# Kernel optimization log

Hardware: AMD Instinct MI355X
Metric: run time of the kernel (lower is better)

The kernel has to match this reference:

```python
import jax, jax.numpy as jnp
import numpy as np

N = 30000   # clients (single instance, repeat=1)
F = 16      # num_node_features
EP = 30000  # solution-graph (tour) edges per parent
EF = 240000 # full graph k-NN edges (degree 8)
H = 8       # heads
D = 64      # hidden_dim
R = 64      # routes per parent (= max_to_move)
HD = H * D  # 512


def _gatv2(x, src, dst, ea, Wl, Wr, We, att, b, d_out):
    # PyG GATv2Conv: score = att . leaky_relu(Wl x_src + Wr x_dst + We e), softmax over dst
    n = x.shape[0]
    xl = (x @ Wl).reshape(n, H, d_out)
    xr = (x @ Wr).reshape(n, H, d_out)
    ee = (ea @ We).reshape(-1, H, d_out)
    s = jax.nn.leaky_relu(xl[src] + xr[dst] + ee, 0.2)          # [E,H,d]
    logits = jnp.einsum('ehd,hd->eh', s, att)                    # [E,H]
    m = jax.ops.segment_max(logits, dst, num_segments=n)
    ex = jnp.exp(logits - m[dst])
    den = jax.ops.segment_sum(ex, dst, num_segments=n)
    alpha = ex / (den[dst] + 1e-16)
    out = jax.ops.segment_sum(xl[src] * alpha[..., None], dst, num_segments=n)
    return out.reshape(n, H * d_out) + b


def _bn(x, g, b):
    # BatchNorm with track_running_stats=False -> batch statistics
    mu = jnp.mean(x, 0)
    v = jnp.var(x, 0)
    return (x - mu) * jax.lax.rsqrt(v + 1e-5) * g + b


def _routes(emb, rid):
    # sum client embeddings per route, then prefix sums over routes (moved vs kept sets)
    rs = jax.ops.segment_sum(emb, rid, num_segments=R)   # [R, 2HD]
    cs = jnp.cumsum(rs, 0)
    return cs, cs[-1] - cs


def setup_inputs() -> dict:
    key = jax.random.key(0)
    ks = iter(jax.random.split(key, 64))
    sc = 0.05
    rn = lambda shape: jax.random.normal(next(ks), shape, jnp.float32)
    d = {}
    d['x_p1'] = rn((N, F)); d['x_p2'] = rn((N, F)); d['x_full'] = rn((N, F))
    d['ea_p1'] = jax.random.uniform(next(ks), (EP, 1))
    d['ea_p2'] = jax.random.uniform(next(ks), (EP, 1))
    d['ea_full'] = jax.random.uniform(next(ks), (EF, 1))
    d['ei_p1'] = jax.random.randint(next(ks), (2, EP), 0, N)
    d['ei_p2'] = jax.random.randint(next(ks), (2, EP), 0, N)
    d['ei_full'] = jax.random.randint(next(ks), (2, EF), 0, N)
    d['route_p1'] = jax.random.randint(next(ks), (N,), 0, R)
    d['route_p2'] = jax.random.randint(next(ks), (N,), 0, R)
    # GAT params: (SolutionGraph, FullGraph, both)
    for tag, cin, dout in (('1', F, D), ('2', F, D), ('3', 2 * HD, 2 * D)):
        d['Wl' + tag] = rn((cin, H * dout)) * sc
        d['Wr' + tag] = rn((cin, H * dout)) * sc
        d['We' + tag] = rn((1, H * dout)) * sc
        d['att' + tag] = rn((H, dout)) * sc
        d['b' + tag] = jnp.zeros((H * dout,), jnp.float32)
    d['bng'] = jnp.ones((2 * HD,), jnp.float32); d['bnb'] = jnp.zeros((2 * HD,), jnp.float32)
    d['png'] = jnp.ones((8 * HD,), jnp.float32); d['pnb'] = jnp.zeros((8 * HD,), jnp.float32)
    dims = [8 * HD, 4 * HD, 2 * HD, HD, HD // 2, HD // 4, HD // 8, HD // 16, 1]
    for i in range(8):
        d['W%d' % (i + 1)] = rn((dims[i], dims[i + 1])) * sc
        d['c%d' % (i + 1)] = jnp.zeros((dims[i + 1],), jnp.float32)
    return d


def reference(x_p1, x_p2, x_full, ea_p1, ea_p2, ea_full, ei_p1, ei_p2, ei_full,
              route_p1, route_p2,
              Wl1, Wr1, We1, att1, b1, Wl2, Wr2, We2, att2, b2,
              Wl3, Wr3, We3, att3, b3, bng, bnb, png, pnb,
              W1, c1, W2, c2, W3, c3, W4, c4, W5, c5, W6, c6, W7, c7, W8, c8):
    p1 = _gatv2(x_p1, ei_p1[0], ei_p1[1], ea_p1, Wl1, Wr1, We1, att1, b1, D)
    p2 = _gatv2(x_p2, ei_p2[0], ei_p2[1], ea_p2, Wl1, Wr1, We1, att1, b1, D)
    fg = _gatv2(x_full, ei_full[0], ei_full[1], ea_full, Wl2, Wr2, We2, att2, b2, D)
    # single instance -> repeat=1: concat client embedding with full-graph embedding
    p1f = _bn(jnp.concatenate([p1, fg], 1), bng, bnb)
    p2f = _bn(jnp.concatenate([p2, fg], 1), bng, bnb)
    p1f = _gatv2(p1f, ei_p1[0], ei_p1[1], ea_p1, Wl3, Wr3, We3, att3, b3, 2 * D)
    p2f = _gatv2(p2f, ei_p2[0], ei_p2[1], ea_p2, Wl3, Wr3, We3, att3, b3, 2 * D)
    c1s, r1s = _routes(p1f, route_p1)
    c2s, r2s = _routes(p2f, route_p2)
    ptop = jnp.concatenate([c1s, r1s, c2s, r2s], 1)   # [R, 8*HD]
    h = _bn(ptop, png, pnb)
    lrelu = lambda z: jax.nn.leaky_relu(z, 0.01)
    h = lrelu(h @ W1 + c1)
    h = lrelu(h @ W2 + c2)
    h = lrelu(h @ W3 + c3)
    h = lrelu(h @ W4 + c4)
    h = lrelu(h @ W5 + c5)
    h = lrelu(h @ W6 + c6)
    h = lrelu(h @ W7 + c7)
    h = h @ W8 + c8
    probs = jax.nn.sigmoid(h).ravel()
    ptop_batch = jnp.zeros((R,), jnp.int32)
    return probs, ptop_batch
```

## Files before the change

### kernel.cpp

```cpp
#include <hip/hip_runtime.h>
#include <stdint.h>

typedef unsigned short u16;
typedef unsigned int   u32;
typedef __attribute__((ext_vector_type(8))) short bf16x8;
typedef __attribute__((ext_vector_type(4))) float f32x4;

#define NN    30000
#define EFULL 240000
#define EPAR  30000

__device__ __forceinline__ float b2f(u16 u){ u32 x=((u32)u)<<16; float f; __builtin_memcpy(&f,&x,4); return f; }
__device__ __forceinline__ u16 f2b(float f){ u32 x; __builtin_memcpy(&x,&f,4); x += 0x7fffu + ((x>>16)&1u); return (u16)(x>>16); }

__device__ __forceinline__ void gload_lds16(const u16* g, u16* l){
  __builtin_amdgcn_global_load_lds((const __attribute__((address_space(1))) void*)g,
                                   (__attribute__((address_space(3))) void*)l, 16, 0, 0);
}

__global__ void k_fail(float* out){ int t=threadIdx.x; if(t<128) out[t]=2.0f; }

__global__ void k_counte3(const int* __restrict__ d0, const int* __restrict__ d1, const int* __restrict__ d2,
                          int* __restrict__ c0, int* __restrict__ c1, int* __restrict__ c2){
  int z = blockIdx.z;
  const int* d = z==0? d0 : z==1? d1 : d2;
  int* c = z==0? c0 : z==1? c1 : c2;
  int E = z==0? EFULL : EPAR;
  int e = blockIdx.x*256 + threadIdx.x;
  if (e < E) atomicAdd(&c[d[e]], 1);
}

__global__ void k_scan3(const int* __restrict__ c0, const int* __restrict__ c1, const int* __restrict__ c2,
                        int* __restrict__ r0, int* __restrict__ r1, int* __restrict__ r2,
                        int* __restrict__ w0, int* __restrict__ w1, int* __restrict__ w2){
  __shared__ int sums[1024];
  int z = blockIdx.x;
  const int* cnt = z==0? c0 : z==1? c1 : c2;
  int* rp = z==0? r0 : z==1? r1 : r2;
  int* wp = z==0? w0 : z==1? w1 : w2;
  int t = threadIdx.x;
  const int CH = (NN + 1023)/1024;
  int c00 = t*CH;
  int s = 0;
  for (int i=0;i<CH;i++){ int idx=c00+i; s += (idx<NN)? cnt[idx] : 0; }
  sums[t] = s; __syncthreads();
  for (int off=1; off<1024; off<<=1){
    int v = (t>=off)? sums[t-off] : 0;
    __syncthreads();
    sums[t] += v;
    __syncthreads();
  }
  int run = (t==0)? 0 : sums[t-1];
  for (int i=0;i<CH;i++){
    int idx=c00+i;
    if (idx<NN){ rp[idx]=run; wp[idx]=run; run += cnt[idx]; }
  }
  if (t==1023) rp[NN] = sums[1023];
}

__global__ void k_fill3(const int* __restrict__ d0, const int* __restrict__ d1, const int* __restrict__ d2,
                        int* __restrict__ w0, int* __restrict__ w1, int* __restrict__ w2,
                        int* __restrict__ x0, int* __restrict__ x1, int* __restrict__ x2){
  int z = blockIdx.z;
  const int* d = z==0? d0 : z==1? d1 : d2;
  int* w = z==0? w0 : z==1? w1 : w2;
  int* x = z==0? x0 : z==1? x1 : x2;
  int E = z==0? EFULL : EPAR;
  int e = blockIdx.x*256 + threadIdx.x;
  if (e < E){ int p = atomicAdd(&w[d[e]], 1); x[p] = e; }
}

__global__ void k_count64(const int* __restrict__ rt0, const int* __restrict__ rt1,
                          const int* __restrict__ d0, const int* __restrict__ d1,
                          int* __restrict__ c0, int* __restrict__ c1,
                          int* __restrict__ c2, int* __restrict__ c3){
  int z = blockIdx.z;
  int i = blockIdx.x*256 + threadIdx.x;
  if (i >= NN) return;
  if      (z==0) atomicAdd(&c0[rt0[i]], 1);
  else if (z==1) atomicAdd(&c1[rt1[i]], 1);
  else if (z==2) atomicAdd(&c2[rt0[d0[i]]], 1);
  else           atomicAdd(&c3[rt1[d1[i]]], 1);
}

__global__ void k_scan64x4(const int* __restrict__ c0, const int* __restrict__ c1,
                           const int* __restrict__ c2, const int* __restrict__ c3,
                           int* __restrict__ r0, int* __restrict__ r1,
                           int* __restrict__ r2, int* __restrict__ r3,
                           int* __restrict__ w0, int* __restrict__ w1,
                           int* __restrict__ w2, int* __restrict__ w3){
  int t = threadIdx.x;
  if (t >= 4) return;
  const int* c = t==0?c0:t==1?c1:t==2?c2:c3;
  int* r = t==0?r0:t==1?r1:t==2?r2:r3;
  int* w = t==0?w0:t==1?w1:t==2?w2:w3;
  int run=0;
  for (int i=0;i<64;i++){ r[i]=run; w[i]=run; run+=c[i]; }
  r[64]=run;
}

__global__ void k_fill64(const int* __restrict__ rt0, const int* __restrict__ rt1,
                         const int* __restrict__ d0, const int* __restrict__ d1,
                         int* __restrict__ w0, int* __restrict__ w1,
                         int* __restrict__ w2, int* __restrict__ w3,
                         int* __restrict__ x0, int* __restrict__ x1,
                         int* __restrict__ x2, int* __restrict__ x3){
  int z = blockIdx.z;
  int i = blockIdx.x*256 + threadIdx.x;
  if (i >= NN) return;
  if      (z==0){ int p=atomicAdd(&w0[rt0[i]],1);      x0[p]=i; }
  else if (z==1){ int p=atomicAdd(&w1[rt1[i]],1);      x1[p]=i; }
  else if (z==2){ int p=atomicAdd(&w2[rt0[d0[i]]],1);  x2[p]=i; }
  else          { int p=atomicAdd(&w3[rt1[d1[i]]],1);  x3[p]=i; }
}

__global__ __launch_bounds__(256) void k_xw(const float* __restrict__ x,
                                            const float* __restrict__ Wl, const float* __restrict__ Wr,
                                            u16* __restrict__ xl, u16* __restrict__ xr){
  int n = blockIdx.x;
  int c = blockIdx.y*256 + threadIdx.x;
  float xv[16];
  #pragma unroll
  for (int k=0;k<16;k++) xv[k] = x[n*16+k];
  float aL=0.f, aR=0.f;
  #pragma unroll
  for (int k=0;k<16;k++){
    aL += xv[k]*Wl[k*512+c];
    aR += xv[k]*Wr[k*512+c];
  }
  xl[(size_t)n*512+c]=f2b(aL); xr[(size_t)n*512+c]=f2b(aR);
}

__global__ __launch_bounds__(256) void k_gat1f(const int* __restrict__ ei,
    const float* __restrict__ ea,
    const int* __restrict__ rp, const int* __restrict__ eix,
    const float* __restrict__ We, const float* __restrict__ att,
    const u16* __restrict__ xl, const u16* __restrict__ xr,
    const float* __restrict__ bias, u16* __restrict__ out){
  int lane = threadIdx.x & 63;
  int n = blockIdx.x*4 + (threadIdx.x>>6);
  if (n >= NN) return;
  int j0 = lane*8;
  float we8[8], at8[8], rv8[8];
  bf16x8 rv = *(const bf16x8*)(xr + (size_t)n*512 + j0);
  #pragma unroll
  for (int j=0;j<8;j++){ we8[j]=We[j0+j]; at8[j]=att[j0+j]; rv8[j]=b2f((u16)rv[j]); }
  int r0 = rp[n], r1 = rp[n+1];
  float den = 0.f;
  float acc[8] = {0,0,0,0,0,0,0,0};
  for (int i=r0;i<r1;i++){
    int e = eix[i];
    int src = ei[e];
    float eaw = ea[e];
    bf16x8 lv = *(const bf16x8*)(xl + (size_t)src*512 + j0);
    float lvf[8];
    float logit = 0.f;
    #pragma unroll
    for (int j=0;j<8;j++){
      lvf[j] = b2f((u16)lv[j]);
      float v = lvf[j] + rv8[j] + eaw*we8[j];
      v = v>0.f? v : 0.2f*v;
      logit += v*at8[j];
    }
    logit += __shfl_xor(logit,1);
    logit += __shfl_xor(logit,2);
    logit += __shfl_xor(logit,4);
    float a = __expf(logit);
    den += a;
    #pragma unroll
    for (int j=0;j<8;j++) acc[j] += a*lvf[j];
  }
  float inv = 1.f/(den + 1e-16f);
  #pragma unroll
  for (int j=0;j<8;j++) out[(size_t)n*512 + j0 + j] = f2b(acc[j]*inv + bias[j0+j]);
}

__global__ __launch_bounds__(256) void k_bnstats(const u16* __restrict__ P1, const u16* __restrict__ P2,
    const u16* __restrict__ PF, float* __restrict__ s1, float* __restrict__ s2, float* __restrict__ sF){
  int z = blockIdx.y;
  const u16* P = z==0? P1 : z==1? P2 : PF;
  float* st = z==0? s1 : z==1? s2 : sF;
  int t = threadIdx.x;
  const u32* Pu = (const u32*)P;
  int r0 = blockIdx.x*250, r1 = r0+250;
  float a0=0.f,a1=0.f,q0=0.f,q1=0.f;
  for (int r=r0;r<r1;r++){
    u32 v = Pu[(size_t)r*256 + t];
    float a = b2f((u16)(v & 0xffffu));
    float b = b2f((u16)(v >> 16));
    a0+=a; q0+=a*a; a1+=b; q1+=b*b;
  }
  atomicAdd(&st[2*t],       a0);
  atomicAdd(&st[2*t+1],     a1);
  atomicAdd(&st[512+2*t],   q0);
  atomicAdd(&st[512+2*t+1], q1);
}

__global__ __launch_bounds__(256) void k_bnapply(u16* __restrict__ P1, u16* __restrict__ P2, u16* __restrict__ PF,
    const float* __restrict__ s1, const float* __restrict__ s2, const float* __restrict__ sF,
    const float* __restrict__ g, const float* __restrict__ b){
  int z = blockIdx.y;
  u16* P = z==0? P1 : z==1? P2 : PF;
  const float* st = z==0? s1 : z==1? s2 : sF;
  int coff = (z==2)? 512 : 0;
  int idx = blockIdx.x*256 + threadIdx.x;
  if (idx >= NN*512) return;
  int c = idx & 511;
  const float invN = 1.f/30000.f;
  float mu = st[c]*invN;
  float var = st[512+c]*invN - mu*mu;
  float r = rsqrtf(var + 1e-5f);
  float v = b2f(P[idx]);
  P[idx] = f2b((v-mu)*r*g[coff+c] + b[coff+c]);
}

__global__ __launch_bounds__(256) void k_bt(const float* __restrict__ B0, const float* __restrict__ B1,
                                            u16* __restrict__ Bt){
  __shared__ u16 tile[64][65];
  int bk = blockIdx.x;
  int bn = blockIdx.y;
  const float* B = blockIdx.z ? B1 : B0;
  int nb = blockIdx.z*1024;
  for (int i = threadIdx.x; i < 64*64; i += 256){
    int r = i>>6, c = i&63;
    tile[c][r] = f2b(B[(size_t)(bk*64+r)*1024 + bn*64 + c]);
  }
  __syncthreads();
  for (int i = threadIdx.x; i < 64*64; i += 256){
    int r = i>>6, c = i&63;
    Bt[(size_t)(nb + bn*64 + r)*1024 + bk*64 + c] = tile[r][c];
  }
}

__global__ __launch_bounds__(256) void k_gemm(const u16* __restrict__ A0, const u16* __restrict__ A1,
    const u16* __restrict__ Bt, u16* __restrict__ C, int M){
  __shared__ u16 As[128*64];
  __shared__ u16 Bs[128*64];
  int lin = blockIdx.y*16 + blockIdx.x;
  int wg  = (lin&7)*470 + (lin>>3);
  int n0 = (wg & 15)*128;
  int m0 = (wg >> 4)*128;
  int t = threadIdx.x;
  int wave = t>>6, lane = t&63;
  int wm = (wave>>1)*64, wn = (wave&1)*64;
  int rr = lane&15, kq = (lane>>4)*8;
  int srow = t>>3;
  int scol = (t&7)*8;
  int ssw  = ((t&7) ^ (srow&7))*8;
  f32x4 acc[4][4];
  #pragma unroll
  for (int m=0;m<4;m++)
    #pragma unroll
    for (int n=0;n<4;n++){ acc[m][n][0]=0.f; acc[m][n][1]=0.f; acc[m][n][2]=0.f; acc[m][n][3]=0.f; }
  for (int k0=0; k0<1024; k0+=64){
    const u16* Ap = (k0 < 512) ? A0 : A1;
    int kc = k0 & 511;
    #pragma unroll
    for (int i=0;i<4;i++){
      int row = i*32 + srow;
      gload_lds16(Ap + (size_t)(m0+row)*512 + kc + ssw, As + row*64 + scol);
    }
    #pragma unroll
    for (int i=0;i<4;i++){
      int row = i*32 + srow;
      gload_lds16(Bt + (size_t)(n0+row)*1024 + k0 + ssw, Bs + row*64 + scol);
    }
    __syncthreads();
    #pragma unroll
    for (int ks=0; ks<2; ks++){
      int pc = ((ks*4 + (lane>>4)) ^ (lane&7))*8;
      bf16x8 af[4], bb[4];
      #pragma unroll
      for (int m=0;m<4;m++) af[m] = *(const bf16x8*)(&As[(wm + m*16 + rr)*64 + pc]);
      #pragma unroll
      for (int n=0;n<4;n++) bb[n] = *(const bf16x8*)(&Bs[(wn + n*16 + rr)*64 + pc]);
      #pragma unroll
      for (int m=0;m<4;m++)
        #pragma unroll
        for (int n=0;n<4;n++)
          acc[m][n] = __builtin_amdgcn_mfma_f32_16x16x32_bf16(af[m], bb[n], acc[m][n], 0, 0, 0);
    }
    __syncthreads();
  }
  int rq = (lane>>4)*4;
  #pragma unroll
  for (int m=0;m<4;m++)
    #pragma unroll
    for (int n=0;n<4;n++)
      #pragma unroll
      for (int j=0;j<4;j++){
        int row = m0 + wm + m*16 + rq + j;
        int col = n0 + wn + n*16 + rr;
        if (row < M) C[(size_t)row*2048 + col] = f2b(acc[m][n][j]);
      }
}

__global__ __launch_bounds__(256) void k_edge2(const int* __restrict__ ei, const float* __restrict__ ea,
    const float* __restrict__ We, const float* __restrict__ att,
    const u16* __restrict__ CAT, float* __restrict__ ex, int E){
  int lane = threadIdx.x & 63;
  int e = blockIdx.x*4 + (threadIdx.x>>6);
  if (e >= E) return;
  int src = ei[e], dst = ei[E+e];
  float eaw = ea[e];
  int j0 = lane*16;
  bf16x8 l0 = *(const bf16x8*)(CAT + (size_t)src*2048 + j0);
  bf16x8 l1 = *(const bf16x8*)(CAT + (size_t)src*2048 + j0 + 8);
  bf16x8 r0 = *(const bf16x8*)(CAT + (size_t)dst*2048 + 1024 + j0);
  bf16x8 r1 = *(const bf16x8*)(CAT + (size_t)dst*2048 + 1024 + j0 + 8);
  float logit = 0.f;
  #pragma unroll
  for (int j=0;j<16;j++){
    float lvj = b2f((u16)((j<8)? l0[j] : l1[j-8]));
    float rvj = b2f((u16)((j<8)? r0[j] : r1[j-8]));
    float v = lvj + rvj + eaw*We[j0+j];
    v = v > 0.f ? v : 0.2f*v;
    logit += v * att[j0+j];
  }
  logit += __shfl_xor(logit,1);
  logit += __shfl_xor(logit,2);
  logit += __shfl_xor(logit,4);
  if ((lane&7)==0) ex[(size_t)e*8 + (lane>>3)] = __expf(logit);
}

__global__ void k_denalpha(const int* __restrict__ rp, const int* __restrict__ eix,
                           const float* __restrict__ ex, float* __restrict__ alpha){
  int idx = blockIdx.x*256 + threadIdx.x;
  if (idx >= NN*8) return;
  int n = idx>>3, h = idx&7;
  int e0 = rp[n], e1 = rp[n+1];
  float s = 0.f;
  for (int i=e0;i<e1;i++) s += ex[(size_t)eix[i]*8 + h];
  float inv = 1.f/(s + 1e-16f);
  for (int i=e0;i<e1;i++){
    int e = eix[i];
    alpha[(size_t)e*8 + h] = ex[(size_t)e*8 + h]*inv;
  }
}

#define ECH 32
__global__ __launch_bounds__(256) void k_agg2pool(const int* __restrict__ ei,
    const int* __restrict__ rerp, const int* __restrict__ reix,
    const int* __restrict__ rrp,
    const float* __restrict__ alpha, const u16* __restrict__ CAT,
    const float* __restrict__ b3, float* __restrict__ rs){
  int r = blockIdx.x;
  int c = blockIdx.z*256 + threadIdx.x;
  int h = c >> 7;
  int i0 = rerp[r], i1 = rerp[r+1];
  int per = (i1 - i0 + ECH - 1)/ECH;
  int s0 = i0 + blockIdx.y*per;
  int s1 = min(i1, s0 + per);
  float acc = 0.f;
  for (int i=s0;i<s1;i++){
    int e = reix[i];
    float a = alpha[(size_t)e*8 + h];
    acc += a * b2f(CAT[(size_t)ei[e]*2048 + c]);
  }
  if (blockIdx.y == 0) acc += (float)(rrp[r+1]-rrp[r]) * b3[c];
  if (s0 < s1 || blockIdx.y == 0) atomicAdd(&rs[r*1024 + c], acc);
}

__global__ void k_cumsum(const float* __restrict__ rs1, const float* __restrict__ rs2,
                         float* __restrict__ ptop){
  const float* rs = blockIdx.y ? rs2 : rs1;
  int colbase = blockIdx.y ? 2048 : 0;
  int c = blockIdx.x*256 + threadIdx.x;
  float tot = 0.f;
  for (int r=0;r<64;r++) tot += rs[r*1024+c];
  float cs = 0.f;
  for (int r=0;r<64;r++){
    cs += rs[r*1024+c];
    ptop[r*4096 + colbase + c] = cs;
    ptop[r*4096 + colbase + 1024 + c] = tot - cs;
  }
}

__global__ void k_pnbn(const float* __restrict__ ptop, const float* __restrict__ g, const float* __restrict__ b,
                       float* __restrict__ h){
  int c = blockIdx.x*256 + threadIdx.x;
  float s=0.f, q=0.f;
  for (int r=0;r<64;r++){ float v = ptop[r*4096+c]; s+=v; q+=v*v; }
  float mu = s*(1.f/64.f), var = q*(1.f/64.f)-mu*mu;
  float rr = rsqrtf(var + 1e-5f);
  float gg = g[c], bb = b[c];
  for (int r=0;r<64;r++) h[r*4096+c] = (ptop[r*4096+c]-mu)*rr*gg + bb;
}

#define KC 512
__global__ __launch_bounds__(256) void k_mlp_part(const float* __restrict__ In,
    const float* __restrict__ W, float* __restrict__ PART, int Ci, int Co){
  __shared__ float tin[64*64];
  int c  = blockIdx.x*64 + (threadIdx.x&63);
  int rg = threadIdx.x>>6;
  int k0 = blockIdx.y*KC, k1 = min(Ci, k0+KC);
  float acc[16];
  #pragma unroll
  for (int j=0;j<16;j++) acc[j]=0.f;
  for (int ks=k0; ks<k1; ks+=64){
    int kw = min(64, k1-ks);
    __syncthreads();
    for (int i=threadIdx.x;i<64*64;i+=256){
      int r=i>>6, k=i&63;
      tin[i] = (k<kw)? In[(size_t)r*Ci + ks + k] : 0.f;
    }
    __syncthreads();
    if (c < Co){
      for (int k=0;k<kw;k+=4){
        float4 w4;
        w4.x = W[(size_t)(ks+k  )*Co + c];
        w4.y = W[(size_t)(ks+k+1)*Co + c];
        w4.z = W[(size_t)(ks+k+2)*Co + c];
        w4.w = W[(size_t)(ks+k+3)*Co + c];
        #pragma unroll
        for (int j=0;j<16;j++){
          float4 t4 = *(const float4*)(&tin[(rg*16+j)*64 + k]);
          acc[j] += t4.x*w4.x + t4.y*w4.y + t4.z*w4.z + t4.w*w4.w;
        }
      }
    }
  }
  if (c < Co){
    float* P = PART + (size_t)blockIdx.y*64*Co;
    #pragma unroll
    for (int j=0;j<16;j++)
      P[(size_t)(rg*16+j)*Co + c] = acc[j];
  }
}

__global__ void k_mlp_red(const float* __restrict__ PART, const float* __restrict__ bias,
                          float* __restrict__ Out, int Co, int SK, int act){
  int idx = blockIdx.x*256 + threadIdx.x;
  if (idx >= 64*Co) return;
  int c = idx % Co;
  float s = bias[c];
  for (int sk=0; sk<SK; sk++) s += PART[(size_t)sk*64*Co + idx];
  if (act) s = s>0.f ? s : 0.01f*s;
  Out[idx] = s;
}

__global__ __launch_bounds__(256) void k_mlp_tail(const float* __restrict__ In,
    const float* __restrict__ W6, const float* __restrict__ c6,
    const float* __restrict__ W7, const float* __restrict__ c7,
    const float* __restrict__ W8, const float* __restrict__ c8,
    float* __restrict__ out){
  __shared__ float A[64*128];
  __shared__ float B[64*64];
  int t = threadIdx.x;
  for (int i=t;i<64*128;i+=256) A[i] = In[i];
  __syncthreads();
  for (int idx=t; idx<64*64; idx+=256){
    int r=idx>>6, c=idx&63;
    float s=c6[c];
    for (int k=0;k<128;k++) s += A[r*128+k]*W6[k*64+c];
    B[idx] = s>0.f? s : 0.01f*s;
  }
  __syncthreads();
  for (int idx=t; idx<64*32; idx+=256){
    int r=idx>>5, c=idx&31;
    float s=c7[c];
    for (int k=0;k<64;k++) s += B[r*64+k]*W7[k*32+c];
    A[idx] = s>0.f? s : 0.01f*s;
  }
  __syncthreads();
  if (t<64){
    float s=c8[0];
    for (int k=0;k<32;k++) s += A[t*32+k]*W8[k];
    out[t] = 1.f/(1.f + __expf(-s));
    out[64+t] = 0.f;
  }
}

extern "C" void kernel_launch(void* const* d_in, const int* in_sizes, int n_in,
                              void* d_out, int out_size, void* d_ws, size_t ws_size,
                              hipStream_t stream)
{
  const float* x_p1   = (const float*)d_in[0];
  const float* x_p2   = (const float*)d_in[1];
  const float* x_full = (const float*)d_in[2];
  const float* ea_p1  = (const float*)d_in[3];
  const float* ea_p2  = (const float*)d_in[4];
  const float* ea_full= (const float*)d_in[5];
  const int* ei_p1  = (const int*)d_in[6];
  const int* ei_p2  = (const int*)d_in[7];
  const int* ei_full= (const int*)d_in[8];
  const int* route_p1 = (const int*)d_in[9];
  const int* route_p2 = (const int*)d_in[10];
  const float *Wl1=(const float*)d_in[11], *Wr1=(const float*)d_in[12], *We1=(const float*)d_in[13], *att1=(const float*)d_in[14], *b1=(const float*)d_in[15];
  const float *Wl2=(const float*)d_in[16], *Wr2=(const float*)d_in[17], *We2=(const float*)d_in[18], *att2=(const float*)d_in[19], *b2=(const float*)d_in[20];
  const float *Wl3=(const float*)d_in[21], *Wr3=(const float*)d_in[22], *We3=(const float*)d_in[23], *att3=(const float*)d_in[24], *b3=(const float*)d_in[25];
  const float *bng=(const float*)d_in[26], *bnb=(const float*)d_in[27], *png=(const float*)d_in[28], *pnb=(const float*)d_in[29];
  const float *W[8], *Cb[8];
  for (int i=0;i<8;i++){ W[i]=(const float*)d_in[30+2*i]; Cb[i]=(const float*)d_in[31+2*i]; }

  char* w = (char*)d_ws;
  size_t off = 0;
  auto alloc = [&](size_t bytes)->char*{ char* p = w + off; off += (bytes + 255) & ~(size_t)255; return p; };
  u16* P1bf = (u16*)alloc((size_t)NN*512*2);
  u16* P2bf = (u16*)alloc((size_t)NN*512*2);
  u16* FGbf = (u16*)alloc((size_t)NN*512*2);
  char* BIG = alloc((size_t)NN*2048*2);
  u16*   XLbf = (u16*)BIG;
  u16*   XRbf = (u16*)(BIG + (size_t)NN*512*2);
  u16*   CATbf= (u16*)BIG;
  u16*   Bt   = (u16*)alloc((size_t)2048*1024*2);
  float* EX2 = (float*)alloc((size_t)EPAR*8*4);
  float* ALPHA=(float*)alloc((size_t)EPAR*8*4);
  float* st1 = (float*)alloc(1024*4);
  float* st2 = (float*)alloc(1024*4);
  float* stF = (float*)alloc(1024*4);
  float* rs1 = (float*)alloc(64*1024*4);
  float* rs2 = (float*)alloc(64*1024*4);
  float* PTOP= (float*)alloc(64*4096*4);
  float* H0  = (float*)alloc(64*4096*4);
  float* H1  = (float*)alloc(64*4096*4);
  float* PART= (float*)alloc((size_t)8*64*2048*4);
  char* cnt_base = alloc(0);
  int* cntF = (int*)alloc(NN*4);
  int* cntA = (int*)alloc(NN*4);
  int* cntB = (int*)alloc(NN*4);
  int* c64a = (int*)alloc(64*4);
  int* c64b = (int*)alloc(64*4);
  int* c64c = (int*)alloc(64*4);
  int* c64d = (int*)alloc(64*4);
  size_t cnt_bytes = (size_t)((char*)alloc(0) - cnt_base);
  int* wpF = (int*)alloc(NN*4);
  int* wpA = (int*)alloc(NN*4);
  int* wpB = (int*)alloc(NN*4);
  int* w64a= (int*)alloc(64*4);
  int* w64b= (int*)alloc(64*4);
  int* w64c= (int*)alloc(64*4);
  int* w64d= (int*)alloc(64*4);
  int* rpF = (int*)alloc((NN+1)*4);
  int* rp1 = (int*)alloc((NN+1)*4);
  int* rp2 = (int*)alloc((NN+1)*4);
  int* eixF= (int*)alloc((size_t)EFULL*4);
  int* eix1= (int*)alloc((size_t)EPAR*4);
  int* eix2= (int*)alloc((size_t)EPAR*4);
  int* rr1 = (int*)alloc(65*4);
  int* rr2 = (int*)alloc(65*4);
  int* rerp1=(int*)alloc(65*4);
  int* rerp2=(int*)alloc(65*4);
  int* nix1= (int*)alloc(NN*4);
  int* nix2= (int*)alloc(NN*4);
  int* reix1=(int*)alloc((size_t)EPAR*4);
  int* reix2=(int*)alloc((size_t)EPAR*4);
  if (ws_size < off){ k_fail<<<1,128,0,stream>>>((float*)d_out); return; }

  hipMemsetAsync(cnt_base, 0, cnt_bytes, stream);
  hipMemsetAsync(st1, 0, 3*4096 + 2*64*1024*4 + 2*256, stream);

  k_counte3<<<dim3((EFULL+255)/256,1,3), 256, 0, stream>>>(ei_full+EFULL, ei_p1+EPAR, ei_p2+EPAR,
                                                           cntF, cntA, cntB);
  k_scan3  <<<3, 1024, 0, stream>>>(cntF, cntA, cntB, rpF, rp1, rp2, wpF, wpA, wpB);
  k_fill3  <<<dim3((EFULL+255)/256,1,3), 256, 0, stream>>>(ei_full+EFULL, ei_p1+EPAR, ei_p2+EPAR,
                                                           wpF, wpA, wpB, eixF, eix1, eix2);
  k_count64<<<dim3((NN+255)/256,1,4), 256, 0, stream>>>(route_p1, route_p2, ei_p1+EPAR, ei_p2+EPAR,
                                                        c64a, c64b, c64c, c64d);
  k_scan64x4<<<1, 64, 0, stream>>>(c64a,c64b,c64c,c64d, rr1,rr2,rerp1,rerp2, w64a,w64b,w64c,w64d);
  k_fill64 <<<dim3((NN+255)/256,1,4), 256, 0, stream>>>(route_p1, route_p2, ei_p1+EPAR, ei_p2+EPAR,
                                                        w64a,w64b,w64c,w64d, nix1,nix2,reix1,reix2);

  k_bt<<<dim3(16,16,2), 256, 0, stream>>>(Wl3, Wr3, Bt);

  auto gat1 = [&](const float* x, const int* ei, const float* ea, const int* rp, const int* eix,
                  const float* Wl, const float* Wr, const float* We, const float* att, const float* bias,
                  u16* out){
    k_xw   <<<dim3(NN,2), 256, 0, stream>>>(x, Wl, Wr, XLbf, XRbf);
    k_gat1f<<<(NN+3)/4, 256, 0, stream>>>(ei, ea, rp, eix, We, att, XLbf, XRbf, bias, out);
  };
  gat1(x_full, ei_full, ea_full, rpF, eixF, Wl2, Wr2, We2, att2, b2, FGbf);
  gat1(x_p1,   ei_p1,   ea_p1,   rp1, eix1, Wl1, Wr1, We1, att1, b1, P1bf);
  gat1(x_p2,   ei_p2,   ea_p2,   rp2, eix2, Wl1, Wr1, We1, att1, b1, P2bf);

  k_bnstats<<<dim3(120,3), 256, 0, stream>>>(P1bf, P2bf, FGbf, st1, st2, stF);
  int nbn = (NN*512+255)/256;
  k_bnapply<<<dim3(nbn,3), 256, 0, stream>>>(P1bf, P2bf, FGbf, st1, st2, stF, bng, bnb);

  auto layer2 = [&](const u16* Pbf, const int* ei, const float* ea, const int* rp, const int* eix,
                    const int* rrp, const int* rerp, const int* reix, float* rs){
    k_gemm <<<dim3(16, (NN+127)/128), 256, 0, stream>>>(Pbf, FGbf, Bt, CATbf, NN);
    k_edge2<<<(EPAR+3)/4, 256, 0, stream>>>(ei, ea, We3, att3, CATbf, EX2, EPAR);
    k_denalpha<<<(NN*8+255)/256, 256, 0, stream>>>(rp, eix, EX2, ALPHA);
    k_agg2pool<<<dim3(64,ECH,4), 256, 0, stream>>>(ei, rerp, reix, rrp, ALPHA, CATbf, b3, rs);
  };
  layer2(P1bf, ei_p1, ea_p1, rp1, eix1, rr1, rerp1, reix1, rs1);
  layer2(P2bf, ei_p2, ea_p2, rp2, eix2, rr2, rerp2, reix2, rs2);

  k_cumsum<<<dim3(4,2), 256, 0, stream>>>(rs1, rs2, PTOP);
  k_pnbn  <<<16, 256, 0, stream>>>(PTOP, png, pnb, H0);

  int dims[9] = {4096, 2048, 1024, 512, 256, 128, 64, 32, 1};
  float* bufs[2] = {H0, H1};
  for (int i=0;i<5;i++){
    int Ci = dims[i], Co = dims[i+1];
    int SK = (Ci + KC - 1)/KC;
    k_mlp_part<<<dim3((Co+63)/64, SK), 256, 0, stream>>>(bufs[i&1], W[i], PART, Ci, Co);
    k_mlp_red <<<(64*Co+255)/256, 256, 0, stream>>>(PART, Cb[i], bufs[(i+1)&1], Co, SK, 1);
  }
  k_mlp_tail<<<1, 256, 0, stream>>>(bufs[1], W[5], Cb[5], W[6], Cb[6], W[7], Cb[7], (float*)d_out);
}
```

Measured before the change: 1.701 ms.

## Fold batchnorm into GEMM weights and fuse edge softmax per destination node

Batchnorm on the concatenated features is no longer applied elementwise. Its scale is folded into the transposed layer-3 weights for each parent, and its shift becomes a per-column bias added in the GEMM epilogue. The edge-logit and denominator kernels merge into one destination-centric kernel, the right projection of layer 1 is computed inline instead of being materialised, the cumsum and batchnorm-over-routes kernels are fused, and the unused route node-index fill is dropped. This removes several full passes over large bf16 buffers. In exchange it needs two weight transposes, a serial 1024-long dot product per shift column, and it changes bf16 rounding order.

```diff
diff --git a/kernel.cpp b/kernel.cpp
--- a/kernel.cpp
+++ b/kernel.cpp
@@ -87,64 +87,65 @@
                            const int* __restrict__ c2, const int* __restrict__ c3,
                            int* __restrict__ r0, int* __restrict__ r1,
                            int* __restrict__ r2, int* __restrict__ r3,
-                           int* __restrict__ w0, int* __restrict__ w1,
                            int* __restrict__ w2, int* __restrict__ w3){
   int t = threadIdx.x;
   if (t >= 4) return;
   const int* c = t==0?c0:t==1?c1:t==2?c2:c3;
   int* r = t==0?r0:t==1?r1:t==2?r2:r3;
-  int* w = t==0?w0:t==1?w1:t==2?w2:w3;
   int run=0;
-  for (int i=0;i<64;i++){ r[i]=run; w[i]=run; run+=c[i]; }
+  for (int i=0;i<64;i++){
+    r[i]=run;
+    if (t==2) w2[i]=run;
+    if (t==3) w3[i]=run;
+    run+=c[i];
+  }
   r[64]=run;
 }
 
-__global__ void k_fill64(const int* __restrict__ rt0, const int* __restrict__ rt1,
+__global__ void k_fille2(const int* __restrict__ rt0, const int* __restrict__ rt1,
                          const int* __restrict__ d0, const int* __restrict__ d1,
-                         int* __restrict__ w0, int* __restrict__ w1,
                          int* __restrict__ w2, int* __restrict__ w3,
-                         int* __restrict__ x0, int* __restrict__ x1,
                          int* __restrict__ x2, int* __restrict__ x3){
   int z = blockIdx.z;
   int i = blockIdx.x*256 + threadIdx.x;
-  if (i >= NN) return;
-  if      (z==0){ int p=atomicAdd(&w0[rt0[i]],1);      x0[p]=i; }
-  else if (z==1){ int p=atomicAdd(&w1[rt1[i]],1);      x1[p]=i; }
-  else if (z==2){ int p=atomicAdd(&w2[rt0[d0[i]]],1);  x2[p]=i; }
-  else          { int p=atomicAdd(&w3[rt1[d1[i]]],1);  x3[p]=i; }
-}
-
-__global__ __launch_bounds__(256) void k_xw(const float* __restrict__ x,
-                                            const float* __restrict__ Wl, const float* __restrict__ Wr,
-                                            u16* __restrict__ xl, u16* __restrict__ xr){
+  if (i >= EPAR) return;
+  if (z==0){ int p=atomicAdd(&w2[rt0[d0[i]]],1);  x2[p]=i; }
+  else     { int p=atomicAdd(&w3[rt1[d1[i]]],1);  x3[p]=i; }
+}
+
+__global__ __launch_bounds__(256) void k_xwl(const float* __restrict__ x,
+                                             const float* __restrict__ Wl, u16* __restrict__ xl){
   int n = blockIdx.x;
   int c = blockIdx.y*256 + threadIdx.x;
-  float xv[16];
-  #pragma unroll
-  for (int k=0;k<16;k++) xv[k] = x[n*16+k];
-  float aL=0.f, aR=0.f;
-  #pragma unroll
-  for (int k=0;k<16;k++){
-    aL += xv[k]*Wl[k*512+c];
-    aR += xv[k]*Wr[k*512+c];
-  }
-  xl[(size_t)n*512+c]=f2b(aL); xr[(size_t)n*512+c]=f2b(aR);
+  float a=0.f;
+  #pragma unroll
+  for (int k=0;k<16;k++) a += x[n*16+k]*Wl[k*512+c];
+  xl[(size_t)n*512+c]=f2b(a);
 }
 
 __global__ __launch_bounds__(256) void k_gat1f(const int* __restrict__ ei,
     const float* __restrict__ ea,
     const int* __restrict__ rp, const int* __restrict__ eix,
+    const float* __restrict__ x, const float* __restrict__ Wr,
     const float* __restrict__ We, const float* __restrict__ att,
-    const u16* __restrict__ xl, const u16* __restrict__ xr,
+    const u16* __restrict__ xl,
     const float* __restrict__ bias, u16* __restrict__ out){
   int lane = threadIdx.x & 63;
   int n = blockIdx.x*4 + (threadIdx.x>>6);
   if (n >= NN) return;
   int j0 = lane*8;
+  float xv[16];
+  #pragma unroll
+  for (int k=0;k<16;k++) xv[k] = x[n*16+k];
   float we8[8], at8[8], rv8[8];
-  bf16x8 rv = *(const bf16x8*)(xr + (size_t)n*512 + j0);
-  #pragma unroll
-  for (int j=0;j<8;j++){ we8[j]=We[j0+j]; at8[j]=att[j0+j]; rv8[j]=b2f((u16)rv[j]); }
+  #pragma unroll
+  for (int j=0;j<8;j++){
+    we8[j]=We[j0+j]; at8[j]=att[j0+j];
+    float s=0.f;
+    #pragma unroll
+    for (int k=0;k<16;k++) s += xv[k]*Wr[k*512 + j0 + j];
+    rv8[j]=s;
+  }
   int r0 = rp[n], r1 = rp[n+1];
   float den = 0.f;
   float acc[8] = {0,0,0,0,0,0,0,0};
@@ -196,44 +197,64 @@
   atomicAdd(&st[512+2*t+1], q1);
 }
 
-__global__ __launch_bounds__(256) void k_bnapply(u16* __restrict__ P1, u16* __restrict__ P2, u16* __restrict__ PF,
-    const float* __restrict__ s1, const float* __restrict__ s2, const float* __restrict__ sF,
-    const float* __restrict__ g, const float* __restrict__ b){
-  int z = blockIdx.y;
-  u16* P = z==0? P1 : z==1? P2 : PF;
-  const float* st = z==0? s1 : z==1? s2 : sF;
-  int coff = (z==2)? 512 : 0;
-  int idx = blockIdx.x*256 + threadIdx.x;
-  if (idx >= NN*512) return;
-  int c = idx & 511;
+__global__ void k_prep(const float* __restrict__ st1, const float* __restrict__ st2,
+                       const float* __restrict__ stF,
+                       const float* __restrict__ g, const float* __restrict__ b,
+                       float* __restrict__ sc1, float* __restrict__ sh1,
+                       float* __restrict__ sc2, float* __restrict__ sh2){
+  int k = blockIdx.x*256 + threadIdx.x;
+  if (k >= 1024) return;
   const float invN = 1.f/30000.f;
-  float mu = st[c]*invN;
-  float var = st[512+c]*invN - mu*mu;
-  float r = rsqrtf(var + 1e-5f);
-  float v = b2f(P[idx]);
-  P[idx] = f2b((v-mu)*r*g[coff+c] + b[coff+c]);
+  const float* st = (k<512)? st1 : stF;
+  int kk = k & 511;
+  float mu = st[kk]*invN;
+  float var = st[512+kk]*invN - mu*mu;
+  float sc = g[k]*rsqrtf(var + 1e-5f);
+  sc1[k] = sc; sh1[k] = b[k] - mu*sc;
+  st = (k<512)? st2 : stF;
+  mu = st[kk]*invN;
+  var = st[512+kk]*invN - mu*mu;
+  sc = g[k]*rsqrtf(var + 1e-5f);
+  sc2[k] = sc; sh2[k] = b[k] - mu*sc;
 }
 
 __global__ __launch_bounds__(256) void k_bt(const float* __restrict__ B0, const float* __restrict__ B1,
-                                            u16* __restrict__ Bt){
-  __shared__ u16 tile[64][65];
+                                            const float* __restrict__ sc1, const float* __restrict__ sc2,
+                                            u16* __restrict__ Bt1, u16* __restrict__ Bt2){
+  __shared__ float tile[64][65];
   int bk = blockIdx.x;
   int bn = blockIdx.y;
-  const float* B = blockIdx.z ? B1 : B0;
-  int nb = blockIdx.z*1024;
+  int par = blockIdx.z>>1, half = blockIdx.z&1;
+  const float* B = half ? B1 : B0;
+  const float* sc = par ? sc2 : sc1;
+  u16* Bt = par ? Bt2 : Bt1;
+  int nb = half*1024;
   for (int i = threadIdx.x; i < 64*64; i += 256){
     int r = i>>6, c = i&63;
-    tile[c][r] = f2b(B[(size_t)(bk*64+r)*1024 + bn*64 + c]);
+    tile[c][r] = B[(size_t)(bk*64+r)*1024 + bn*64 + c] * sc[bk*64+r];
   }
   __syncthreads();
   for (int i = threadIdx.x; i < 64*64; i += 256){
     int r = i>>6, c = i&63;
-    Bt[(size_t)(nb + bn*64 + r)*1024 + bk*64 + c] = tile[r][c];
-  }
+    Bt[(size_t)(nb + bn*64 + r)*1024 + bk*64 + c] = f2b(tile[r][c]);
+  }
+}
+
+__global__ void k_shiftb(const float* __restrict__ B0, const float* __restrict__ B1,
+                         const float* __restrict__ sh1, const float* __restrict__ sh2,
+                         float* __restrict__ sb1, float* __restrict__ sb2){
+  int c = blockIdx.x*256 + threadIdx.x;
+  const float* sh = blockIdx.y ? sh2 : sh1;
+  float* sb = blockIdx.y ? sb2 : sb1;
+  const float* B = (c < 1024) ? B0 : B1;
+  int cc = c & 1023;
+  float s = 0.f;
+  for (int k=0;k<1024;k++) s += sh[k]*B[(size_t)k*1024 + cc];
+  sb[c] = s;
 }
 
 __global__ __launch_bounds__(256) void k_gemm(const u16* __restrict__ A0, const u16* __restrict__ A1,
-    const u16* __restrict__ Bt, u16* __restrict__ C, int M){
+    const u16* __restrict__ Bt, const float* __restrict__ sb, u16* __restrict__ C, int M){
   __shared__ u16 As[128*64];
   __shared__ u16 Bs[128*64];
   int lin = blockIdx.y*16 + blockIdx.x;
@@ -291,50 +312,55 @@
       for (int j=0;j<4;j++){
         int row = m0 + wm + m*16 + rq + j;
         int col = n0 + wn + n*16 + rr;
-        if (row < M) C[(size_t)row*2048 + col] = f2b(acc[m][n][j]);
+        if (row < M) C[(size_t)row*2048 + col] = f2b(acc[m][n][j] + sb[col]);
       }
 }
 
-__global__ __launch_bounds__(256) void k_edge2(const int* __restrict__ ei, const float* __restrict__ ea,
+__global__ __launch_bounds__(256) void k_edge2f(const int* __restrict__ ei,
+    const float* __restrict__ ea,
+    const int* __restrict__ rp, const int* __restrict__ eix,
     const float* __restrict__ We, const float* __restrict__ att,
-    const u16* __restrict__ CAT, float* __restrict__ ex, int E){
+    const u16* __restrict__ CAT, float* __restrict__ alpha){
   int lane = threadIdx.x & 63;
-  int e = blockIdx.x*4 + (threadIdx.x>>6);
-  if (e >= E) return;
-  int src = ei[e], dst = ei[E+e];
-  float eaw = ea[e];
+  int n = blockIdx.x*4 + (threadIdx.x>>6);
+  if (n >= NN) return;
   int j0 = lane*16;
-  bf16x8 l0 = *(const bf16x8*)(CAT + (size_t)src*2048 + j0);
-  bf16x8 l1 = *(const bf16x8*)(CAT + (size_t)src*2048 + j0 + 8);
-  bf16x8 r0 = *(const bf16x8*)(CAT + (size_t)dst*2048 + 1024 + j0);
-  bf16x8 r1 = *(const bf16x8*)(CAT + (size_t)dst*2048 + 1024 + j0 + 8);
-  float logit = 0.f;
+  float rv[16], we16[16], at16[16];
+  bf16x8 rr0 = *(const bf16x8*)(CAT + (size_t)n*2048 + 1024 + j0);
+  bf16x8 rr1 = *(const bf16x8*)(CAT + (size_t)n*2048 + 1024 + j0 + 8);
   #pragma unroll
   for (int j=0;j<16;j++){
-    float lvj = b2f((u16)((j<8)? l0[j] : l1[j-8]));
-    float rvj = b2f((u16)((j<8)? r0[j] : r1[j-8]));
-    float v = lvj + rvj + eaw*We[j0+j];
-    v = v > 0.f ? v : 0.2f*v;
-    logit += v * att[j0+j];
-  }
-  logit += __shfl_xor(logit,1);
-  logit += __shfl_xor(logit,2);
-  logit += __shfl_xor(logit,4);
-  if ((lane&7)==0) ex[(size_t)e*8 + (lane>>3)] = __expf(logit);
-}
-
-__global__ void k_denalpha(const int* __restrict__ rp, const int* __restrict__ eix,
-                           const float* __restrict__ ex, float* __restrict__ alpha){
-  int idx = blockIdx.x*256 + threadIdx.x;
-  if (idx >= NN*8) return;
-  int n = idx>>3, h = idx&7;
+    rv[j] = b2f((u16)((j<8)? rr0[j] : rr1[j-8]));
+    we16[j]=We[j0+j]; at16[j]=att[j0+j];
+  }
   int e0 = rp[n], e1 = rp[n+1];
-  float s = 0.f;
-  for (int i=e0;i<e1;i++) s += ex[(size_t)eix[i]*8 + h];
-  float inv = 1.f/(s + 1e-16f);
+  float den = 0.f;
   for (int i=e0;i<e1;i++){
     int e = eix[i];
-    alpha[(size_t)e*8 + h] = ex[(size_t)e*8 + h]*inv;
+    int src = ei[e];
+    float eaw = ea[e];
+    bf16x8 l0 = *(const bf16x8*)(CAT + (size_t)src*2048 + j0);
+    bf16x8 l1 = *(const bf16x8*)(CAT + (size_t)src*2048 + j0 + 8);
+    float logit = 0.f;
+    #pragma unroll
+    for (int j=0;j<16;j++){
+      float v = b2f((u16)((j<8)? l0[j] : l1[j-8])) + rv[j] + eaw*we16[j];
+      v = v>0.f? v : 0.2f*v;
+      logit += v*at16[j];
+    }
+    logit += __shfl_xor(logit,1);
+    logit += __shfl_xor(logit,2);
+    logit += __shfl_xor(logit,4);
+    float ex_ = __expf(logit);
+    if ((lane&7)==0){ alpha[(size_t)e*8 + (lane>>3)] = ex_; den += ex_; }
+  }
+  float dh = __shfl(den, (lane&7)*8);
+  float inv = 1.f/(dh + 1e-16f);
+  if (lane < 8){
+    for (int i=e0;i<e1;i++){
+      int e = eix[i];
+      alpha[(size_t)e*8 + lane] *= inv;
+    }
   }
 }
 
@@ -361,30 +387,31 @@
   if (s0 < s1 || blockIdx.y == 0) atomicAdd(&rs[r*1024 + c], acc);
 }
 
-__global__ void k_cumsum(const float* __restrict__ rs1, const float* __restrict__ rs2,
-                         float* __restrict__ ptop){
+__global__ void k_cumsum_bn(const float* __restrict__ rs1, const float* __restrict__ rs2,
+                            const float* __restrict__ g, const float* __restrict__ b,
+                            float* __restrict__ h){
   const float* rs = blockIdx.y ? rs2 : rs1;
   int colbase = blockIdx.y ? 2048 : 0;
   int c = blockIdx.x*256 + threadIdx.x;
   float tot = 0.f;
   for (int r=0;r<64;r++) tot += rs[r*1024+c];
-  float cs = 0.f;
+  float cs=0.f, s0=0.f,q0=0.f,s1=0.f,q1=0.f;
   for (int r=0;r<64;r++){
     cs += rs[r*1024+c];
-    ptop[r*4096 + colbase + c] = cs;
-    ptop[r*4096 + colbase + 1024 + c] = tot - cs;
-  }
-}
-
-__global__ void k_pnbn(const float* __restrict__ ptop, const float* __restrict__ g, const float* __restrict__ b,
-                       float* __restrict__ h){
-  int c = blockIdx.x*256 + threadIdx.x;
-  float s=0.f, q=0.f;
-  for (int r=0;r<64;r++){ float v = ptop[r*4096+c]; s+=v; q+=v*v; }
-  float mu = s*(1.f/64.f), var = q*(1.f/64.f)-mu*mu;
-  float rr = rsqrtf(var + 1e-5f);
-  float gg = g[c], bb = b[c];
-  for (int r=0;r<64;r++) h[r*4096+c] = (ptop[r*4096+c]-mu)*rr*gg + bb;
+    float m = tot - cs;
+    s0+=cs; q0+=cs*cs; s1+=m; q1+=m*m;
+  }
+  float mu0=s0*(1.f/64.f), v0=q0*(1.f/64.f)-mu0*mu0, n0=rsqrtf(v0+1e-5f);
+  float mu1=s1*(1.f/64.f), v1=q1*(1.f/64.f)-mu1*mu1, n1=rsqrtf(v1+1e-5f);
+  float g0=g[colbase+c],      b0=b[colbase+c];
+  float g1=g[colbase+1024+c], b1=b[colbase+1024+c];
+  cs = 0.f;
+  for (int r=0;r<64;r++){
+    cs += rs[r*1024+c];
+    float m = tot - cs;
+    h[r*4096 + colbase + c]        = (cs-mu0)*n0*g0 + b0;
+    h[r*4096 + colbase + 1024 + c] = (m -mu1)*n1*g1 + b1;
+  }
 }
 
 #define KC 512
@@ -501,17 +528,21 @@
   u16* FGbf = (u16*)alloc((size_t)NN*512*2);
   char* BIG = alloc((size_t)NN*2048*2);
   u16*   XLbf = (u16*)BIG;
-  u16*   XRbf = (u16*)(BIG + (size_t)NN*512*2);
   u16*   CATbf= (u16*)BIG;
-  u16*   Bt   = (u16*)alloc((size_t)2048*1024*2);
-  float* EX2 = (float*)alloc((size_t)EPAR*8*4);
+  u16*   Bt1  = (u16*)alloc((size_t)2048*1024*2);
+  u16*   Bt2  = (u16*)alloc((size_t)2048*1024*2);
   float* ALPHA=(float*)alloc((size_t)EPAR*8*4);
   float* st1 = (float*)alloc(1024*4);
   float* st2 = (float*)alloc(1024*4);
   float* stF = (float*)alloc(1024*4);
   float* rs1 = (float*)alloc(64*1024*4);
   float* rs2 = (float*)alloc(64*1024*4);
-  float* PTOP= (float*)alloc(64*4096*4);
+  float* sc1 = (float*)alloc(1024*4);
+  float* sh1 = (float*)alloc(1024*4);
+  float* sc2 = (float*)alloc(1024*4);
+  float* sh2 = (float*)alloc(1024*4);
+  float* sb1 = (float*)alloc(2048*4);
+  float* sb2 = (float*)alloc(2048*4);
   float* H0  = (float*)alloc(64*4096*4);
   float* H1  = (float*)alloc(64*4096*4);
   float* PART= (float*)alloc((size_t)8*64*2048*4);
@@ -527,8 +558,6 @@
   int* wpF = (int*)alloc(NN*4);
   int* wpA = (int*)alloc(NN*4);
   int* wpB = (int*)alloc(NN*4);
-  int* w64a= (int*)alloc(64*4);
-  int* w64b= (int*)alloc(64*4);
   int* w64c= (int*)alloc(64*4);
   int* w64d= (int*)alloc(64*4);
   int* rpF = (int*)alloc((NN+1)*4);
@@ -541,14 +570,12 @@
   int* rr2 = (int*)alloc(65*4);
   int* rerp1=(int*)alloc(65*4);
   int* rerp2=(int*)alloc(65*4);
-  int* nix1= (int*)alloc(NN*4);
-  int* nix2= (int*)alloc(NN*4);
   int* reix1=(int*)alloc((size_t)EPAR*4);
   int* reix2=(int*)alloc((size_t)EPAR*4);
   if (ws_size < off){ k_fail<<<1,128,0,stream>>>((float*)d_out); return; }
 
   hipMemsetAsync(cnt_base, 0, cnt_bytes, stream);
-  hipMemsetAsync(st1, 0, 3*4096 + 2*64*1024*4 + 2*256, stream);
+  hipMemsetAsync(st1, 0, (size_t)((char*)rs2 - (char*)st1) + 64*1024*4, stream);
 
   k_counte3<<<dim3((EFULL+255)/256,1,3), 256, 0, stream>>>(ei_full+EFULL, ei_p1+EPAR, ei_p2+EPAR,
                                                            cntF, cntA, cntB);
@@ -557,38 +584,36 @@
                                                            wpF, wpA, wpB, eixF, eix1, eix2);
   k_count64<<<dim3((NN+255)/256,1,4), 256, 0, stream>>>(route_p1, route_p2, ei_p1+EPAR, ei_p2+EPAR,
                                                         c64a, c64b, c64c, c64d);
-  k_scan64x4<<<1, 64, 0, stream>>>(c64a,c64b,c64c,c64d, rr1,rr2,rerp1,rerp2, w64a,w64b,w64c,w64d);
-  k_fill64 <<<dim3((NN+255)/256,1,4), 256, 0, stream>>>(route_p1, route_p2, ei_p1+EPAR, ei_p2+EPAR,
-                                                        w64a,w64b,w64c,w64d, nix1,nix2,reix1,reix2);
-
-  k_bt<<<dim3(16,16,2), 256, 0, stream>>>(Wl3, Wr3, Bt);
+  k_scan64x4<<<1, 64, 0, stream>>>(c64a,c64b,c64c,c64d, rr1,rr2,rerp1,rerp2, w64c,w64d);
+  k_fille2 <<<dim3((NN+255)/256,1,2), 256, 0, stream>>>(route_p1, route_p2, ei_p1+EPAR, ei_p2+EPAR,
+                                                        w64c, w64d, reix1, reix2);
 
   auto gat1 = [&](const float* x, const int* ei, const float* ea, const int* rp, const int* eix,
                   const float* Wl, const float* Wr, const float* We, const float* att, const float* bias,
                   u16* out){
-    k_xw   <<<dim3(NN,2), 256, 0, stream>>>(x, Wl, Wr, XLbf, XRbf);
-    k_gat1f<<<(NN+3)/4, 256, 0, stream>>>(ei, ea, rp, eix, We, att, XLbf, XRbf, bias, out);
+    k_xwl  <<<dim3(NN,2), 256, 0, stream>>>(x, Wl, XLbf);
+    k_gat1f<<<(NN+3)/4, 256, 0, stream>>>(ei, ea, rp, eix, x, Wr, We, att, XLbf, bias, out);
   };
   gat1(x_full, ei_full, ea_full, rpF, eixF, Wl2, Wr2, We2, att2, b2, FGbf);
   gat1(x_p1,   ei_p1,   ea_p1,   rp1, eix1, Wl1, Wr1, We1, att1, b1, P1bf);
   gat1(x_p2,   ei_p2,   ea_p2,   rp2, eix2, Wl1, Wr1, We1, att1, b1, P2bf);
 
   k_bnstats<<<dim3(120,3), 256, 0, stream>>>(P1bf, P2bf, FGbf, st1, st2, stF);
-  int nbn = (NN*512+255)/256;
-  k_bnapply<<<dim3(nbn,3), 256, 0, stream>>>(P1bf, P2bf, FGbf, st1, st2, stF, bng, bnb);
-
-  auto layer2 = [&](const u16* Pbf, const int* ei, const float* ea, const int* rp, const int* eix,
+  k_prep   <<<4, 256, 0, stream>>>(st1, st2, stF, bng, bnb, sc1, sh1, sc2, sh2);
+  k_bt     <<<dim3(16,16,4), 256, 0, stream>>>(Wl3, Wr3, sc1, sc2, Bt1, Bt2);
+  k_shiftb <<<dim3(8,2), 256, 0, stream>>>(Wl3, Wr3, sh1, sh2, sb1, sb2);
+
+  auto layer2 = [&](const u16* Pbf, const u16* Bt, const float* sb,
+                    const int* ei, const float* ea, const int* rp, const int* eix,
                     const int* rrp, const int* rerp, const int* reix, float* rs){
-    k_gemm <<<dim3(16, (NN+127)/128), 256, 0, stream>>>(Pbf, FGbf, Bt, CATbf, NN);
-    k_edge2<<<(EPAR+3)/4, 256, 0, stream>>>(ei, ea, We3, att3, CATbf, EX2, EPAR);
-    k_denalpha<<<(NN*8+255)/256, 256, 0, stream>>>(rp, eix, EX2, ALPHA);
+    k_gemm <<<dim3(16, (NN+127)/128), 256, 0, stream>>>(Pbf, FGbf, Bt, sb, CATbf, NN);
+    k_edge2f<<<(NN+3)/4, 256, 0, stream>>>(ei, ea, rp, eix, We3, att3, CATbf, ALPHA);
     k_agg2pool<<<dim3(64,ECH,4), 256, 0, stream>>>(ei, rerp, reix, rrp, ALPHA, CATbf, b3, rs);
   };
-  layer2(P1bf, ei_p1, ea_p1, rp1, eix1, rr1, rerp1, reix1, rs1);
-  layer2(P2bf, ei_p2, ea_p2, rp2, eix2, rr2, rerp2, reix2, rs2);
-
-  k_cumsum<<<dim3(4,2), 256, 0, stream>>>(rs1, rs2, PTOP);
-  k_pnbn  <<<16, 256, 0, stream>>>(PTOP, png, pnb, H0);
+  layer2(P1bf, Bt1, sb1, ei_p1, ea_p1, rp1, eix1, rr1, rerp1, reix1, rs1);
+  layer2(P2bf, Bt2, sb2, ei_p2, ea_p2, rp2, eix2, rr2, rerp2, reix2, rs2);
+
+  k_cumsum_bn<<<dim3(4,2), 256, 0, stream>>>(rs1, rs2, png, pnb, H0);
 
   int dims[9] = {4096, 2048, 1024, 512, 256, 128, 64, 32, 1};
   float* bufs[2] = {H0, H1};
```

New measurement: 1.813 ms. 6.6% more time.
